# Performance work log

Hardware: AMD Instinct MI355X
Metric: run time of the kernel (lower is better)

The kernel has to match this reference:

```python
import jax, jax.numpy as jnp
import numpy as np

N_NODES = 50000
DEG = 32
N_EDGES = N_NODES * DEG
IN_DIM = 256
HID = 64
OUT = 64
N_CLASSES = 40
N_GRAPHS = 64
NEG_SLOPE = 0.2


def setup_inputs() -> dict:
    key = jax.random.key(0)
    ks = jax.random.split(key, 12)
    h = jax.random.normal(ks[0], (N_NODES, IN_DIM), dtype=jnp.float32)
    # every node has exactly DEG incoming edges -> dst sorted, no zero in-degree
    dst = jnp.repeat(jnp.arange(N_NODES, dtype=jnp.int32), DEG)
    src = jax.random.randint(ks[1], (N_EDGES,), 0, N_NODES, dtype=jnp.int32)
    # evenly sized graphs so mean_nodes never divides by zero
    graph_ids = (jnp.arange(N_NODES, dtype=jnp.int32) * N_GRAPHS) // N_NODES
    s1 = 1.0 / np.sqrt(IN_DIM)
    s2 = 1.0 / np.sqrt(HID)
    W1 = jax.random.normal(ks[2], (IN_DIM, HID), jnp.float32) * s1
    al1 = jax.random.normal(ks[3], (HID,), jnp.float32) * s2
    ar1 = jax.random.normal(ks[4], (HID,), jnp.float32) * s2
    b1 = jnp.zeros((HID,), jnp.float32)
    W2 = jax.random.normal(ks[5], (HID, OUT), jnp.float32) * s2
    al2 = jax.random.normal(ks[6], (OUT,), jnp.float32) / np.sqrt(OUT)
    ar2 = jax.random.normal(ks[7], (OUT,), jnp.float32) / np.sqrt(OUT)
    b2 = jnp.zeros((OUT,), jnp.float32)
    p_drop = jnp.full((HID,), 0.5, jnp.float32)  # VariationalDropout retain probs
    Wc = jax.random.normal(ks[8], (OUT, N_CLASSES), jnp.float32) / np.sqrt(OUT)
    bc = jnp.zeros((N_CLASSES,), jnp.float32)
    return {"h": h, "src": src, "dst": dst, "graph_ids": graph_ids,
            "n_graphs": N_GRAPHS, "W1": W1, "al1": al1, "ar1": ar1, "b1": b1,
            "W2": W2, "al2": al2, "ar2": ar2, "b2": b2,
            "p_drop": p_drop, "Wc": Wc, "bc": bc}


def _gat_conv(h, W, al, ar, b, src, dst, n_nodes):
    f = h @ W                                  # [N, d]
    el = f @ al                                # [N]
    er = f @ ar                                # [N]
    e = jax.nn.leaky_relu(el[src] + er[dst], NEG_SLOPE)   # [E]
    m = jax.ops.segment_max(e, dst, num_segments=n_nodes, indices_are_sorted=True)
    ex = jnp.exp(e - m[dst])
    s = jax.ops.segment_sum(ex, dst, num_segments=n_nodes, indices_are_sorted=True)
    alpha = ex / s[dst]                        # edge softmax over incoming edges
    out = jax.ops.segment_sum(alpha[:, None] * f[src], dst,
                              num_segments=n_nodes, indices_are_sorted=True)
    return out + b


def reference(h, src, dst, graph_ids, n_graphs, W1, al1, ar1, b1,
              W2, al2, ar2, b2, p_drop, Wc, bc):
    n_nodes = h.shape[0]
    x = jax.nn.elu(_gat_conv(h, W1, al1, ar1, b1, src, dst, n_nodes))
    x = x * jnp.clip(p_drop, 0.0, 1.0)[None, :]          # deterministic var-dropout
    x = _gat_conv(x, W2, al2, ar2, b2, src, dst, n_nodes)
    # dgl.mean_nodes
    sums = jax.ops.segment_sum(x, graph_ids, num_segments=n_graphs, indices_are_sorted=True)
    cnts = jax.ops.segment_sum(jnp.ones((n_nodes,), x.dtype), graph_ids,
                               num_segments=n_graphs, indices_are_sorted=True)
    hg = sums / cnts[:, None]
    return hg @ Wc + bc
```

## Files before the change

### kernel.cpp

```cpp
#include <hip/hip_runtime.h>
#include <hip/hip_bf16.h>

#define N_NODES   50000
#define DEG       32
#define IN_DIM    256
#define HID       64
#define OUTD      64
#define N_CLASSES 40
#define N_GRAPHS  64

typedef __attribute__((ext_vector_type(8))) short bf16x8;
typedef __attribute__((ext_vector_type(4))) float f32x4;

__device__ __forceinline__ float readlane_f(float v, int l) {
  return __uint_as_float(__builtin_amdgcn_readlane(__float_as_uint(v), l));
}

__device__ __forceinline__ unsigned short f2bf(float f) {
  unsigned int u = __float_as_uint(f);
  return (unsigned short)((u + 0x7fffu + ((u >> 16) & 1u)) >> 16);
}

__device__ __forceinline__ float2 bf2_to_f2(unsigned int v) {
  float2 r;
  r.x = __uint_as_float(v << 16);
  r.y = __uint_as_float(v & 0xffff0000u);
  return r;
}

template<int K_DIM>
__global__ __launch_bounds__(256)
void gemm_heads_mfma(const float* __restrict__ A, const float* __restrict__ W,
                     const float* __restrict__ al, const float* __restrict__ ar,
                     unsigned short* __restrict__ Fb, float* __restrict__ el,
                     float* __restrict__ er, int n_rows)
{
  constexpr int KP = K_DIM + 8;
  __shared__ __align__(16) unsigned short Wt[64 * KP];

  {
    constexpr int ITER = K_DIM * 64 / 1024;
    #pragma unroll
    for (int i = 0; i < ITER; ++i) {
      const int idx4 = threadIdx.x * 4 + i * 1024;
      const int k = idx4 >> 6;
      const int c = idx4 & 63;
      const float4 w = *reinterpret_cast<const float4*>(&W[idx4]);
      Wt[(c + 0) * KP + k] = f2bf(w.x);
      Wt[(c + 1) * KP + k] = f2bf(w.y);
      Wt[(c + 2) * KP + k] = f2bf(w.z);
      Wt[(c + 3) * KP + k] = f2bf(w.w);
    }
  }
  __syncthreads();

  const int lane = threadIdx.x & 63;
  const int wv   = threadIdx.x >> 6;
  const int c    = lane & 15;
  const int g    = lane >> 4;
  const int row0 = blockIdx.x * 64 + wv * 16;

  const long arow = min(row0 + c, n_rows - 1);
  const int  kq   = g * 8;

  f32x4 acc[4];
  #pragma unroll
  for (int nt = 0; nt < 4; ++nt) acc[nt] = (f32x4){0.f, 0.f, 0.f, 0.f};

  #pragma unroll
  for (int ks = 0; ks < K_DIM / 32; ++ks) {
    const float4 q0 = *reinterpret_cast<const float4*>(&A[arow * K_DIM + ks * 32 + kq]);
    const float4 q1 = *reinterpret_cast<const float4*>(&A[arow * K_DIM + ks * 32 + kq + 4]);
    union { bf16x8 v; unsigned short u[8]; } af;
    af.u[0] = f2bf(q0.x); af.u[1] = f2bf(q0.y); af.u[2] = f2bf(q0.z); af.u[3] = f2bf(q0.w);
    af.u[4] = f2bf(q1.x); af.u[5] = f2bf(q1.y); af.u[6] = f2bf(q1.z); af.u[7] = f2bf(q1.w);
    #pragma unroll
    for (int nt = 0; nt < 4; ++nt) {
      const bf16x8 bf =
          *reinterpret_cast<const bf16x8*>(&Wt[(nt * 16 + c) * KP + ks * 32 + kq]);
      acc[nt] = __builtin_amdgcn_mfma_f32_16x16x32_bf16(af.v, bf, acc[nt], 0, 0, 0);
    }
  }

  #pragma unroll
  for (int nt = 0; nt < 4; ++nt) {
    #pragma unroll
    for (int r = 0; r < 4; ++r) {
      const int row = row0 + g * 4 + r;
      if (row < n_rows) Fb[(long)row * 64 + nt * 16 + c] = f2bf(acc[nt][r]);
    }
  }

  float alc[4], arc[4];
  #pragma unroll
  for (int nt = 0; nt < 4; ++nt) { alc[nt] = al[nt * 16 + c]; arc[nt] = ar[nt * 16 + c]; }

  float pe[4], pr[4];
  #pragma unroll
  for (int r = 0; r < 4; ++r) {
    pe[r] = acc[0][r] * alc[0] + acc[1][r] * alc[1] + acc[2][r] * alc[2] + acc[3][r] * alc[3];
    pr[r] = acc[0][r] * arc[0] + acc[1][r] * arc[1] + acc[2][r] * arc[2] + acc[3][r] * arc[3];
  }
  #pragma unroll
  for (int d = 1; d < 16; d <<= 1) {
    #pragma unroll
    for (int r = 0; r < 4; ++r) {
      pe[r] += __shfl_xor(pe[r], d);
      pr[r] += __shfl_xor(pr[r], d);
    }
  }
  if (c == 0) {
    #pragma unroll
    for (int r = 0; r < 4; ++r) {
      const int row = row0 + g * 4 + r;
      if (row < n_rows) { el[row] = pe[r]; er[row] = pr[r]; }
    }
  }
}

template<int MODE>
__global__ __launch_bounds__(256)
void agg_kernel(const unsigned int* __restrict__ F2,
                const float* __restrict__ el, const float* __restrict__ er,
                const int* __restrict__ src, const float* __restrict__ bias,
                const float* __restrict__ pd, float* __restrict__ X, int n_pairs)
{
  const int wid  = (blockIdx.x * 256 + threadIdx.x) >> 6;
  const int lane = threadIdx.x & 63;
  if (wid >= n_pairs) return;
  const int half = lane >> 5;
  const int l32  = lane & 31;
  const int node = wid * 2 + half;

  const int s = src[wid * 64 + lane];
  float ev = el[s] + er[node];
  ev = ev > 0.f ? ev : 0.2f * ev;

  float m = ev;
  #pragma unroll
  for (int d = 16; d; d >>= 1) m = fmaxf(m, __shfl_xor(m, d));
  const float p = __expf(ev - m);
  float sum = p;
  #pragma unroll
  for (int d = 16; d; d >>= 1) sum += __shfl_xor(sum, d);
  const float alpha = p / sum;

  float ax = 0.f, ay = 0.f;
  #pragma unroll
  for (int t = 0; t < 32; ++t) {
    const int   svA = __builtin_amdgcn_readlane(s, t);
    const int   svB = __builtin_amdgcn_readlane(s, t + 32);
    const float aA  = readlane_f(alpha, t);
    const float aB  = readlane_f(alpha, t + 32);
    const int   sv  = half ? svB : svA;
    const float av  = half ? aB : aA;
    const float2 vf = bf2_to_f2(F2[(long)sv * 32 + l32]);
    ax = fmaf(av, vf.x, ax);
    ay = fmaf(av, vf.y, ay);
  }

  float ox = ax + bias[l32 * 2];
  float oy = ay + bias[l32 * 2 + 1];
  if (MODE == 1) {
    ox = ox > 0.f ? ox : (__expf(ox) - 1.f);
    oy = oy > 0.f ? oy : (__expf(oy) - 1.f);
    ox *= fminf(fmaxf(pd[l32 * 2], 0.f), 1.f);
    oy *= fminf(fmaxf(pd[l32 * 2 + 1], 0.f), 1.f);
  }
  reinterpret_cast<float2*>(X)[(long)node * 32 + l32] = make_float2(ox, oy);
}

__global__ __launch_bounds__(256)
void partial_pool_kernel(const float* __restrict__ X2, float* __restrict__ sums)
{
  const int wv   = (blockIdx.x * 256 + threadIdx.x) >> 6;
  const int lane = threadIdx.x & 63;
  if (wv >= N_NODES / 16) return;
  const int base = wv * 16;

  float accR = 0.f;
  int   gcur = (base * 64) / N_NODES;
  #pragma unroll 4
  for (int n = 0; n < 16; ++n) {
    const int i = base + n;
    const int g = (i * 64) / N_NODES;
    if (g != gcur) {
      atomicAdd(&sums[gcur * 64 + lane], accR);
      accR = 0.f; gcur = g;
    }
    accR += X2[(long)i * 64 + lane];
  }
  atomicAdd(&sums[gcur * 64 + lane], accR);
}

__global__ __launch_bounds__(64)
void classify_kernel(const float* __restrict__ sums, const float* __restrict__ Wc,
                     const float* __restrict__ bc, float* __restrict__ out)
{
  const int g     = blockIdx.x;
  const int start = (g * N_NODES + N_GRAPHS - 1) / N_GRAPHS;
  const int end   = ((g + 1) * N_NODES + N_GRAPHS - 1) / N_GRAPHS;
  const int t     = threadIdx.x;

  __shared__ float hg[64];
  hg[t] = sums[g * 64 + t] / (float)(end - start);
  __syncthreads();
  if (t < N_CLASSES) {
    float o = bc[t];
    #pragma unroll
    for (int j = 0; j < 64; ++j) o = fmaf(hg[j], Wc[j * N_CLASSES + t], o);
    out[g * N_CLASSES + t] = o;
  }
}

extern "C" void kernel_launch(void* const* d_in, const int* in_sizes, int n_in,
                              void* d_out, int out_size, void* d_ws, size_t ws_size,
                              hipStream_t stream)
{
  const float* h   = (const float*)d_in[0];
  const int*   src = (const int*)d_in[1];
  const float* W1  = (const float*)d_in[5];
  const float* al1 = (const float*)d_in[6];
  const float* ar1 = (const float*)d_in[7];
  const float* b1  = (const float*)d_in[8];
  const float* W2  = (const float*)d_in[9];
  const float* al2 = (const float*)d_in[10];
  const float* ar2 = (const float*)d_in[11];
  const float* b2  = (const float*)d_in[12];
  const float* pd  = (const float*)d_in[13];
  const float* Wc  = (const float*)d_in[14];
  const float* bc  = (const float*)d_in[15];
  float* out = (float*)d_out;

  float*          ws   = (float*)d_ws;
  float*          xbuf = ws;
  unsigned short* Fb   = (unsigned short*)(ws + 3200000);
  float*          elb  = ws + 4800000;
  float*          erb  = elb + 50000;
  float*          sums = erb + 50000;

  hipMemsetAsync(sums, 0, N_GRAPHS * 64 * sizeof(float), stream);

  gemm_heads_mfma<IN_DIM><<<(N_NODES + 63) / 64, 256, 0, stream>>>(
      h, W1, al1, ar1, Fb, elb, erb, N_NODES);
  agg_kernel<1><<<(N_NODES / 2) / 4, 256, 0, stream>>>(
      (const unsigned int*)Fb, elb, erb, src, b1, pd, xbuf, N_NODES / 2);

  gemm_heads_mfma<HID><<<(N_NODES + 63) / 64, 256, 0, stream>>>(
      xbuf, W2, al2, ar2, Fb, elb, erb, N_NODES);
  agg_kernel<2><<<(N_NODES / 2) / 4, 256, 0, stream>>>(
      (const unsigned int*)Fb, elb, erb, src, b2, pd, xbuf, N_NODES / 2);

  partial_pool_kernel<<<(N_NODES / 16 + 3) / 4, 256, 0, stream>>>(xbuf, sums);
  classify_kernel<<<N_GRAPHS, 64, 0, stream>>>(sums, Wc, bc, out);
}
```

Measured before the change: 198.8 us.

## Split feature table into column halves and aggregate each half in separate passes

The GEMM now writes the bf16 feature matrix as two 32-column halves in separate buffers. Aggregation runs as two kernels per layer, each gathering only one half. Inside each kernel, 16 lanes cover a 64-byte row and two edges are gathered at once, then combined with a shuffle. The aim is to shrink the gathered working set per pass so it fits better in cache, at the cost of recomputing the edge softmax twice, extra launches, and half the lanes idling at the store.

```diff
diff --git a/kernel.cpp b/kernel.cpp
--- a/kernel.cpp
+++ b/kernel.cpp
@@ -32,8 +32,8 @@
 __global__ __launch_bounds__(256)
 void gemm_heads_mfma(const float* __restrict__ A, const float* __restrict__ W,
                      const float* __restrict__ al, const float* __restrict__ ar,
-                     unsigned short* __restrict__ Fb, float* __restrict__ el,
-                     float* __restrict__ er, int n_rows)
+                     unsigned short* __restrict__ Flo, unsigned short* __restrict__ Fhi,
+                     float* __restrict__ el, float* __restrict__ er, int n_rows)
 {
   constexpr int KP = K_DIM + 8;
   __shared__ __align__(16) unsigned short Wt[64 * KP];
@@ -84,10 +84,12 @@
 
   #pragma unroll
   for (int nt = 0; nt < 4; ++nt) {
+    unsigned short* Ft = (nt < 2) ? Flo : Fhi;
+    const int colh = (nt & 1) * 16 + c;
     #pragma unroll
     for (int r = 0; r < 4; ++r) {
       const int row = row0 + g * 4 + r;
-      if (row < n_rows) Fb[(long)row * 64 + nt * 16 + c] = f2bf(acc[nt][r]);
+      if (row < n_rows) Ft[(long)row * 32 + colh] = f2bf(acc[nt][r]);
     }
   }
 
@@ -118,19 +120,19 @@
   }
 }
 
-template<int MODE>
+template<int MODE, int HALF>
 __global__ __launch_bounds__(256)
-void agg_kernel(const unsigned int* __restrict__ F2,
-                const float* __restrict__ el, const float* __restrict__ er,
-                const int* __restrict__ src, const float* __restrict__ bias,
-                const float* __restrict__ pd, float* __restrict__ X, int n_pairs)
+void agg_half_kernel(const unsigned int* __restrict__ Fh,
+                     const float* __restrict__ el, const float* __restrict__ er,
+                     const int* __restrict__ src, const float* __restrict__ bias,
+                     const float* __restrict__ pd, float* __restrict__ X, int n_pairs)
 {
   const int wid  = (blockIdx.x * 256 + threadIdx.x) >> 6;
   const int lane = threadIdx.x & 63;
   if (wid >= n_pairs) return;
-  const int half = lane >> 5;
+  const int h    = lane >> 5;
   const int l32  = lane & 31;
-  const int node = wid * 2 + half;
+  const int node = wid * 2 + h;
 
   const int s = src[wid * 64 + lane];
   float ev = el[s] + er[node];
@@ -145,29 +147,45 @@
   for (int d = 16; d; d >>= 1) sum += __shfl_xor(sum, d);
   const float alpha = p / sum;
 
+  const int sub = l32 >> 4;
+  const int w   = l32 & 15;
+
   float ax = 0.f, ay = 0.f;
   #pragma unroll
-  for (int t = 0; t < 32; ++t) {
-    const int   svA = __builtin_amdgcn_readlane(s, t);
-    const int   svB = __builtin_amdgcn_readlane(s, t + 32);
-    const float aA  = readlane_f(alpha, t);
-    const float aB  = readlane_f(alpha, t + 32);
-    const int   sv  = half ? svB : svA;
-    const float av  = half ? aB : aA;
-    const float2 vf = bf2_to_f2(F2[(long)sv * 32 + l32]);
+  for (int t = 0; t < 16; ++t) {
+    const int   sA0 = __builtin_amdgcn_readlane(s, 2 * t);
+    const int   sA1 = __builtin_amdgcn_readlane(s, 2 * t + 1);
+    const int   sB0 = __builtin_amdgcn_readlane(s, 2 * t + 32);
+    const int   sB1 = __builtin_amdgcn_readlane(s, 2 * t + 33);
+    const float aA0 = readlane_f(alpha, 2 * t);
+    const float aA1 = readlane_f(alpha, 2 * t + 1);
+    const float aB0 = readlane_f(alpha, 2 * t + 32);
+    const float aB1 = readlane_f(alpha, 2 * t + 33);
+    const int   svA = sub ? sA1 : sA0;
+    const int   svB = sub ? sB1 : sB0;
+    const int   sv  = h ? svB : svA;
+    const float avA = sub ? aA1 : aA0;
+    const float avB = sub ? aB1 : aB0;
+    const float av  = h ? avB : avA;
+    const float2 vf = bf2_to_f2(Fh[(long)sv * 16 + w]);
     ax = fmaf(av, vf.x, ax);
     ay = fmaf(av, vf.y, ay);
   }
-
-  float ox = ax + bias[l32 * 2];
-  float oy = ay + bias[l32 * 2 + 1];
-  if (MODE == 1) {
-    ox = ox > 0.f ? ox : (__expf(ox) - 1.f);
-    oy = oy > 0.f ? oy : (__expf(oy) - 1.f);
-    ox *= fminf(fmaxf(pd[l32 * 2], 0.f), 1.f);
-    oy *= fminf(fmaxf(pd[l32 * 2 + 1], 0.f), 1.f);
-  }
-  reinterpret_cast<float2*>(X)[(long)node * 32 + l32] = make_float2(ox, oy);
+  ax += __shfl_xor(ax, 16);
+  ay += __shfl_xor(ay, 16);
+
+  if (sub == 0) {
+    const int col = HALF * 32 + 2 * w;
+    float ox = ax + bias[col];
+    float oy = ay + bias[col + 1];
+    if (MODE == 1) {
+      ox = ox > 0.f ? ox : (__expf(ox) - 1.f);
+      oy = oy > 0.f ? oy : (__expf(oy) - 1.f);
+      ox *= fminf(fmaxf(pd[col], 0.f), 1.f);
+      oy *= fminf(fmaxf(pd[col + 1], 0.f), 1.f);
+    }
+    *reinterpret_cast<float2*>(&X[(long)node * 64 + col]) = make_float2(ox, oy);
+  }
 }
 
 __global__ __launch_bounds__(256)
@@ -234,7 +252,8 @@
 
   float*          ws   = (float*)d_ws;
   float*          xbuf = ws;
-  unsigned short* Fb   = (unsigned short*)(ws + 3200000);
+  unsigned short* Flo  = (unsigned short*)(ws + 3200000);
+  unsigned short* Fhi  = (unsigned short*)(ws + 4000000);
   float*          elb  = ws + 4800000;
   float*          erb  = elb + 50000;
   float*          sums = erb + 50000;
@@ -242,14 +261,18 @@
   hipMemsetAsync(sums, 0, N_GRAPHS * 64 * sizeof(float), stream);
 
   gemm_heads_mfma<IN_DIM><<<(N_NODES + 63) / 64, 256, 0, stream>>>(
-      h, W1, al1, ar1, Fb, elb, erb, N_NODES);
-  agg_kernel<1><<<(N_NODES / 2) / 4, 256, 0, stream>>>(
-      (const unsigned int*)Fb, elb, erb, src, b1, pd, xbuf, N_NODES / 2);
+      h, W1, al1, ar1, Flo, Fhi, elb, erb, N_NODES);
+  agg_half_kernel<1, 0><<<(N_NODES / 2) / 4, 256, 0, stream>>>(
+      (const unsigned int*)Flo, elb, erb, src, b1, pd, xbuf, N_NODES / 2);
+  agg_half_kernel<1, 1><<<(N_NODES / 2) / 4, 256, 0, stream>>>(
+      (const unsigned int*)Fhi, elb, erb, src, b1, pd, xbuf, N_NODES / 2);
 
   gemm_heads_mfma<HID><<<(N_NODES + 63) / 64, 256, 0, stream>>>(
-      xbuf, W2, al2, ar2, Fb, elb, erb, N_NODES);
-  agg_kernel<2><<<(N_NODES / 2) / 4, 256, 0, stream>>>(
-      (const unsigned int*)Fb, elb, erb, src, b2, pd, xbuf, N_NODES / 2);
+      xbuf, W2, al2, ar2, Flo, Fhi, elb, erb, N_NODES);
+  agg_half_kernel<2, 0><<<(N_NODES / 2) / 4, 256, 0, stream>>>(
+      (const unsigned int*)Flo, elb, erb, src, b2, pd, xbuf, N_NODES / 2);
+  agg_half_kernel<2, 1><<<(N_NODES / 2) / 4, 256, 0, stream>>>(
+      (const unsigned int*)Fhi, elb, erb, src, b2, pd, xbuf, N_NODES / 2);
 
   partial_pool_kernel<<<(N_NODES / 16 + 3) / 4, 256, 0, stream>>>(xbuf, sums);
   classify_kernel<<<N_GRAPHS, 64, 0, stream>>>(sums, Wc, bc, out);
```

After: 237.1 us. 1.19x slower.
